# Kernel tuning notes

Measured on AMD Instinct MI355X. Metric: run time of the kernel, lower is better.

## Reference

```python
import jax, jax.numpy as jnp
import numpy as np


def setup_inputs() -> dict:
    key = jax.random.key(0)
    ks = jax.random.split(key, 9)
    b, t_q, t_k, n_q, n_k = 4, 128, 512, 512, 512
    out_size = 512
    s = 0.02  # small init scale for weights
    return {
        "query": jax.random.normal(ks[0], (b, t_q, n_q), jnp.float32),
        "keys": jax.random.normal(ks[1], (b, t_k, n_k), jnp.float32),
        "values": jax.random.normal(ks[2], (b, t_k, n_k), jnp.float32),
        "W_q": jax.random.normal(ks[3], (n_k, n_q), jnp.float32) * s,
        "b_q": jnp.zeros((n_k,), jnp.float32),
        "w_att": jax.random.normal(ks[4], (n_k,), jnp.float32) * s,
        "b_att": jnp.zeros((1,), jnp.float32),
        "W_out": jax.random.normal(ks[5], (out_size, n_q + n_k), jnp.float32) * s,
        "b_out": jnp.zeros((out_size,), jnp.float32),
    }


def reference(query, keys, values, W_q, b_q, w_att, b_att, W_out, b_out):
    # linear_q: [b, t_q, query_size] -> [b, t_q, key_size]
    att_query = jnp.einsum("bqd,nd->bqn", query, W_q) + b_q
    # Bahdanau additive score: tanh(q + k) projected by linear_att (key_size -> 1)
    # intermediate: [b, t_q, t_k, n]
    sum_qk = jnp.tanh(att_query[:, :, None, :] + keys[:, None, :, :])
    scores = jnp.einsum("bqkn,n->bqk", sum_qk, w_att) + b_att[0]
    # mask is None by default; dropout p=0 -> identity
    probs = jax.nn.softmax(scores, axis=-1)  # [b, t_q, t_k]
    context = jnp.einsum("bqk,bkn->bqn", probs, values)
    # linear_out on concat([query, context]) + tanh nonlinearity
    cat = jnp.concatenate([query, context], axis=-1)
    out = jnp.tanh(jnp.einsum("bqc,oc->bqo", cat, W_out) + b_out)
    return out, probs
```

## Files before the change

kernel.cpp:

```cpp
#include <hip/hip_runtime.h>
#include <hip/hip_fp16.h>


#define BB    4
#define TQ    128
#define TK    512
#define NN    512
#define OUTSZ 512
#define CATSZ 1024
#define K2E   2.8853900817779268f
#define L2E   1.4426950408889634f
#define MAT   262144
#define WS_HALVES (15 * MAT)

typedef __attribute__((ext_vector_type(4))) _Float16 half4;
typedef __attribute__((ext_vector_type(8))) _Float16 half8;
typedef __attribute__((ext_vector_type(2))) _Float16 h2;

#if __has_builtin(__builtin_amdgcn_exp2f)
#define EXP2F(x) __builtin_amdgcn_exp2f(x)
#else
#define EXP2F(x) exp2f(x)
#endif
#if __has_builtin(__builtin_amdgcn_rcpf)
#define RCPF(x) __builtin_amdgcn_rcpf(x)
#else
#define RCPF(x) (1.0f / (x))
#endif

__device__ __forceinline__ h2 u2h(unsigned int u) {
  union { unsigned int i; h2 h; } v; v.i = u; return v.h;
}
__device__ __forceinline__ half4 uu2h4(unsigned int a, unsigned int b) {
  union { uint2 u; half4 h; } c; c.u = make_uint2(a, b); return c.h;
}
#if __has_builtin(__builtin_amdgcn_fdot2)
__device__ __forceinline__ float FDOT2(h2 a, h2 b, float c) {
  return __builtin_amdgcn_fdot2(a, b, c, false);
}
#else
__device__ __forceinline__ float FDOT2(h2 a, h2 b, float c) {
  return fmaf((float)a.x, (float)b.x, fmaf((float)a.y, (float)b.y, c));
}
#endif

__device__ __forceinline__ float fast_tanh(float x) {
  float e = EXP2F(x * K2E);
  return fmaf(-2.0f, RCPF(e + 1.0f), 1.0f);
}
__device__ __forceinline__ float waveRedSum(float s) {
  #pragma unroll
  for (int m = 32; m >= 1; m >>= 1) s += __shfl_xor(s, m, 64);
  return s;
}
__device__ __forceinline__ float fma4(float4 w, float4 v, float acc) {
  acc = fmaf(w.x, v.x, acc); acc = fmaf(w.y, v.y, acc);
  acc = fmaf(w.z, v.z, acc); acc = fmaf(w.w, v.w, acc);
  return acc;
}
__device__ __forceinline__ float4 scqh(float4 s, half4 E, float A, float w) {
  s.x = fmaf(w, RCPF(fmaf((float)E.x, A, 1.0f)), s.x);
  s.y = fmaf(w, RCPF(fmaf((float)E.y, A, 1.0f)), s.y);
  s.z = fmaf(w, RCPF(fmaf((float)E.z, A, 1.0f)), s.z);
  s.w = fmaf(w, RCPF(fmaf((float)E.w, A, 1.0f)), s.w);
  return s;
}
__device__ __forceinline__ void dotq(float4& r0, float4& r1, uint4 wp, unsigned int cpa, unsigned int cpb) {
  h2 c0 = u2h(cpa), c1 = u2h(cpb);
  r0.x = FDOT2(u2h(wp.x), c0, r0.x); r1.x = FDOT2(u2h(wp.x), c1, r1.x);
  r0.y = FDOT2(u2h(wp.y), c0, r0.y); r1.y = FDOT2(u2h(wp.y), c1, r1.y);
  r0.z = FDOT2(u2h(wp.z), c0, r0.z); r1.z = FDOT2(u2h(wp.z), c1, r1.z);
  r0.w = FDOT2(u2h(wp.w), c0, r0.w); r1.w = FDOT2(u2h(wp.w), c1, r1.w);
}

__global__ __launch_bounds__(256)
void pack_kernel(const float* __restrict__ query,
                 const float* __restrict__ keys, const float* __restrict__ W_q,
                 const float* __restrict__ W_out, const float* __restrict__ values,
                 _Float16* __restrict__ ws)
{
  __shared__ float tile[32][33];
  const int idx = blockIdx.x;
  const int tx = threadIdx.x & 31, ty = threadIdx.x >> 5;

  if (idx >= 2816) {
    int p = idx - 2816;
    int b = (p & 7) >> 1;
    int qg = ((p >> 3) << 1) | (p & 1);
    const float* q0 = query + ((size_t)(b * TQ + qg * 2)) * NN;
    const float* q1 = q0 + NN;
    int cp = threadIdx.x;
    float2 a = *(const float2*)(q0 + 2 * cp);
    float2 c = *(const float2*)(q1 + 2 * cp);
    half4 h = {(_Float16)a.x, (_Float16)a.y, (_Float16)c.x, (_Float16)c.y};
    *(half4*)(ws + (size_t)11 * MAT + (size_t)p * 2048 + 4 * cp) = h;
    return;
  }

  if (idx >= 1792) {
    int r = idx - 1792;
    int b = r >> 8, k2 = r & 255;
    const float* r0 = values + ((size_t)b * 512 + 2 * k2) * 512;
    const float* r1 = r0 + 512;
    int n0 = threadIdx.x * 2;
    float2 a = *(const float2*)(r0 + n0);
    float2 c = *(const float2*)(r1 + n0);
    _Float16* dst = ws + (size_t)7 * MAT + (size_t)b * MAT + k2 * 1024 + n0 * 2;
    half4 h = {(_Float16)a.x, (_Float16)c.x, (_Float16)a.y, (_Float16)c.y};
    *(half4*)dst = h;
    return;
  }

  if (idx < 1024) {
    int b = idx >> 8, r = idx & 255;
    int by = r >> 4, bx = r & 15;
    const float* src = keys + (size_t)b * MAT;
    _Float16* dst = ws + (size_t)b * MAT;
    #pragma unroll
    for (int i = 0; i < 32; i += 8)
      tile[ty + i][tx] = src[(size_t)(by * 32 + ty + i) * 512 + bx * 32 + tx] * K2E;
    __syncthreads();
    #pragma unroll
    for (int i = 0; i < 32; i += 8)
      dst[(size_t)(bx * 32 + ty + i) * 512 + by * 32 + tx] = (_Float16)EXP2F(tile[tx][ty + i]);
    return;
  }

  const float* src; _Float16* dst; int N; int by, bx;
  if (idx < 1280) {
    int r = idx - 1024; by = r >> 4; bx = r & 15;
    src = W_q; dst = ws + (size_t)4 * MAT; N = 512;
  } else {
    int r = idx - 1280; by = r >> 5; bx = r & 31;
    src = W_out; dst = ws + (size_t)5 * MAT; N = 1024;
  }
  #pragma unroll
  for (int i = 0; i < 32; i += 8)
    tile[ty + i][tx] = src[(size_t)(by * 32 + ty + i) * N + bx * 32 + tx];
  __syncthreads();
  #pragma unroll
  for (int i = 0; i < 32; i += 8) {
    int d = bx * 32 + ty + i;
    int o = by * 32 + tx;
    dst[(size_t)(d >> 1) * 1024 + o * 2 + (d & 1)] = (_Float16)tile[tx][ty + i];
  }
}

__global__ __launch_bounds__(1024, 4)
void attq_kernel(const float* __restrict__ b_q, const float* __restrict__ w_att,
                 _Float16* __restrict__ ws)
{
  __shared__ __align__(16) _Float16 ldsQ[4][1024];
  __shared__ __align__(16) float pt[8][4][2][128];

  const _Float16* wsWqP = ws + (size_t)4 * MAT;
  const _Float16* catG  = ws + (size_t)11 * MAT;
  _Float16* pawG        = ws + (size_t)13 * MAT;

  const int t = threadIdx.x, bx = blockIdx.x;
  const int ng = bx & 3, pg = bx >> 2;

  if (t < 512) {
    int qp = t >> 7, j = t & 127;
    ((uint4*)&ldsQ[qp][0])[j] =
        ((const uint4*)(catG + (size_t)(4 * pg + qp) * 2048))[j];
  }
  __syncthreads();

  const int G = t >> 7, pq = (t >> 5) & 3, v5 = t & 31;
  {
    const _Float16* wq = wsWqP + 8 * (32 * ng + v5);
    float4 a0 = {0,0,0,0}, a1 = {0,0,0,0};
    #pragma unroll 2
    for (int j2 = 0; j2 < 32; j2 += 2) {
      int d2 = 32 * G + j2;
      uint4 wp0 = *(const uint4*)(wq + (size_t)d2 * 1024);
      uint4 wp1 = *(const uint4*)(wq + (size_t)(d2 + 1) * 1024);
      uint4 cp2 = *(const uint4*)(&ldsQ[pq][d2 * 4]);
      dotq(a0, a1, wp0, cp2.x, cp2.y);
      dotq(a0, a1, wp1, cp2.z, cp2.w);
    }
    *(float4*)(&pt[G][pq][0][4 * v5]) = a0;
    *(float4*)(&pt[G][pq][1][4 * v5]) = a1;
  }
  __syncthreads();
  {
    int pq2 = t >> 8, row = (t >> 7) & 1, no = t & 127;
    int n = 128 * ng + no;
    float s = pt[0][pq2][row][no] + pt[1][pq2][row][no]
            + pt[2][pq2][row][no] + pt[3][pq2][row][no]
            + pt[4][pq2][row][no] + pt[5][pq2][row][no]
            + pt[6][pq2][row][no] + pt[7][pq2][row][no];
    float A = EXP2F(K2E * (s + b_q[n]));
    _Float16* dst = pawG + (size_t)(4 * pg + pq2) * 2048 + 4 * n;
    dst[row] = (_Float16)A;
    if (row == 0) {
      dst[2] = (_Float16)w_att[n];
      dst[3] = (_Float16)0.f;
    }
  }
}

__global__ __launch_bounds__(1024, 4)
void attn_mid(_Float16* __restrict__ ws, float* __restrict__ probs)
{
  __shared__ __align__(16) _Float16 pawF[NN * 4];
  __shared__ __align__(16) _Float16 prH[1024];
  __shared__ __align__(16) float  pt[8][2][NN];
  __shared__ float reds2[2][8];

  _Float16* ptH = (_Float16*)pt;

  const _Float16* wsKeys = ws;
  const _Float16* wsValP = ws + (size_t)7 * MAT;
  _Float16* catG         = ws + (size_t)11 * MAT;
  const _Float16* pawG   = ws + (size_t)13 * MAT;

  const int t    = threadIdx.x;
  const int qh   = t >> 9;
  const int u    = t & 511;
  const int G    = t >> 7;
  const int v    = t & 127;
  const int G16  = t >> 6;
  const int v6   = t & 63;
  const int wave = t >> 6, lane = t & 63, wq8 = wave & 7;

  const int p  = blockIdx.x;
  const int b  = (p & 7) >> 1;
  const int qg = ((p >> 3) << 1) | (p & 1);
  const int qabs0 = qg * 2;

  ((unsigned int*)pawF)[t] = ((const unsigned int*)(pawG + (size_t)p * 2048))[t];
  __syncthreads();

  {
    const _Float16* ke = wsKeys + (size_t)b * MAT + 8 * v6;
    float4 s0a = {0,0,0,0}, s0b = {0,0,0,0};
    float4 s1a = {0,0,0,0}, s1b = {0,0,0,0};
    #pragma unroll 2
    for (int j = 0; j < 32; j += 2) {
      int n = 32 * G16 + j;
      uint4 Eu0 = *(const uint4*)(ke + (size_t)n * 512);
      uint4 Eu1 = *(const uint4*)(ke + (size_t)(n + 1) * 512);
      uint4 pw  = *(const uint4*)(&pawF[n * 4]);
      h2 Aab = u2h(pw.x);  float w0f = (float)u2h(pw.y).x;
      h2 Acd = u2h(pw.z);  float w1f = (float)u2h(pw.w).x;
      float A0n = (float)Aab.x, A1n = (float)Aab.y;
      float A0m = (float)Acd.x, A1m = (float)Acd.y;
      half4 E0lo = uu2h4(Eu0.x, Eu0.y), E0hi = uu2h4(Eu0.z, Eu0.w);
      half4 E1lo = uu2h4(Eu1.x, Eu1.y), E1hi = uu2h4(Eu1.z, Eu1.w);
      s0a = scqh(s0a, E0lo, A0n, w0f);
      s0b = scqh(s0b, E0hi, A0n, w0f);
      s1a = scqh(s1a, E0lo, A1n, w0f);
      s1b = scqh(s1b, E0hi, A1n, w0f);
      s0a = scqh(s0a, E1lo, A0m, w1f);
      s0b = scqh(s0b, E1hi, A0m, w1f);
      s1a = scqh(s1a, E1lo, A1m, w1f);
      s1b = scqh(s1b, E1hi, A1m, w1f);
    }
    half8 w0 = {(_Float16)s0a.x, (_Float16)s0a.y, (_Float16)s0a.z, (_Float16)s0a.w,
                (_Float16)s0b.x, (_Float16)s0b.y, (_Float16)s0b.z, (_Float16)s0b.w};
    half8 w1 = {(_Float16)s1a.x, (_Float16)s1a.y, (_Float16)s1a.z, (_Float16)s1a.w,
                (_Float16)s1b.x, (_Float16)s1b.y, (_Float16)s1b.z, (_Float16)s1b.w};
    *(half8*)(ptH + (size_t)G16 * 512 + 8 * v6)        = w0;
    *(half8*)(ptH + 8192 + (size_t)G16 * 512 + 8 * v6) = w1;
  }
  __syncthreads();

  {
    const _Float16* pp = ptH + qh * 8192 + u;
    float s = 0.f;
    #pragma unroll
    for (int g = 0; g < 16; ++g)
      s += (float)pp[g * 512];
    float e = EXP2F(-K2E * s);
    float se = waveRedSum(e);
    if (lane == 0) reds2[qh][wq8] = se;
    __syncthreads();
    float bs = reds2[qh][0]+reds2[qh][1]+reds2[qh][2]+reds2[qh][3]
             + reds2[qh][4]+reds2[qh][5]+reds2[qh][6]+reds2[qh][7];
    float pv = e * RCPF(bs);
    prH[(u >> 1) * 4 + qh * 2 + (u & 1)] = (_Float16)pv;
    probs[((size_t)(b * TQ + qabs0 + qh)) * TK + u] = pv;
  }
  __syncthreads();

  {
    const _Float16* vp = wsValP + (size_t)b * MAT + 8 * v;
    float4 c0 = {0,0,0,0}, c1 = {0,0,0,0};
    #pragma unroll 2
    for (int j2 = 0; j2 < 32; j2 += 2) {
      int k2 = 32 * G + j2;
      uint4 vk0 = *(const uint4*)(vp + (size_t)k2 * 1024);
      uint4 vk1 = *(const uint4*)(vp + (size_t)(k2 + 1) * 1024);
      uint4 pp2 = *(const uint4*)(&prH[k2 * 4]);
      dotq(c0, c1, vk0, pp2.x, pp2.y);
      dotq(c0, c1, vk1, pp2.z, pp2.w);
    }
    *(float4*)(&pt[G][0][4 * v]) = c0;
    *(float4*)(&pt[G][1][4 * v]) = c1;
  }
  __syncthreads();
  {
    float s = pt[0][qh][u] + pt[1][qh][u] + pt[2][qh][u] + pt[3][qh][u]
            + pt[4][qh][u] + pt[5][qh][u] + pt[6][qh][u] + pt[7][qh][u];
    catG[(size_t)p * 2048 + (size_t)(256 + (u >> 1)) * 4 + qh * 2 + (u & 1)] =
        (_Float16)s;
  }
}

__global__ __launch_bounds__(1024, 4)
void out_kernel(const float* __restrict__ b_out, const _Float16* __restrict__ ws,
                float* __restrict__ out)
{
  __shared__ __align__(16) _Float16 ldsCat[8192];
  __shared__ __align__(16) float pt[8][4][2][128];

  const _Float16* wsWoutP = ws + (size_t)5 * MAT;
  const _Float16* catG    = ws + (size_t)11 * MAT;

  const int t = threadIdx.x, bx = blockIdx.x;
  const int og = bx & 3, pg = bx >> 2;

  ((uint4*)ldsCat)[t] = ((const uint4*)(catG + (size_t)4 * pg * 2048))[t];
  __syncthreads();

  const int G = t >> 7, pq = (t >> 5) & 3, v5 = t & 31;
  {
    const _Float16* wo = wsWoutP + 8 * (32 * og + v5);
    float4 o0 = {0,0,0,0}, o1 = {0,0,0,0};
    #pragma unroll 2
    for (int j2 = 0; j2 < 64; j2 += 2) {
      int c2 = 64 * G + j2;
      uint4 wp0 = *(const uint4*)(wo + (size_t)c2 * 1024);
      uint4 wp1 = *(const uint4*)(wo + (size_t)(c2 + 1) * 1024);
      uint4 cp2 = *(const uint4*)(&ldsCat[pq * 2048 + c2 * 4]);
      dotq(o0, o1, wp0, cp2.x, cp2.y);
      dotq(o0, o1, wp1, cp2.z, cp2.w);
    }
    *(float4*)(&pt[G][pq][0][4 * v5]) = o0;
    *(float4*)(&pt[G][pq][1][4 * v5]) = o1;
  }
  __syncthreads();
  {
    int pq2 = t >> 8, row = (t >> 7) & 1, oo = t & 127;
    float s = pt[0][pq2][row][oo] + pt[1][pq2][row][oo]
            + pt[2][pq2][row][oo] + pt[3][pq2][row][oo]
            + pt[4][pq2][row][oo] + pt[5][pq2][row][oo]
            + pt[6][pq2][row][oo] + pt[7][pq2][row][oo];
    int o = 128 * og + oo;
    int p = 4 * pg + pq2;
    int b = (p & 7) >> 1;
    int qg = ((p >> 3) << 1) | (p & 1);
    out[((size_t)(b * TQ + qg * 2 + row)) * OUTSZ + o] = fast_tanh(s + b_out[o]);
  }
}

__device__ __forceinline__ float sc4f(float4 w, float4 k, float4 a, float acc) {
  acc = fmaf(w.x, RCPF(EXP2F(fmaf(k.x, K2E, a.x)) + 1.0f), acc);
  acc = fmaf(w.y, RCPF(EXP2F(fmaf(k.y, K2E, a.y)) + 1.0f), acc);
  acc = fmaf(w.z, RCPF(EXP2F(fmaf(k.z, K2E, a.z)) + 1.0f), acc);
  acc = fmaf(w.w, RCPF(EXP2F(fmaf(k.w, K2E, a.w)) + 1.0f), acc);
  return acc;
}

__global__ __launch_bounds__(1024, 4)
void attn_fallback(const float* __restrict__ query, const float* __restrict__ keys,
                   const float* __restrict__ values, const float* __restrict__ W_q,
                   const float* __restrict__ b_q, const float* __restrict__ w_att,
                   const float* __restrict__ b_att, const float* __restrict__ W_out,
                   const float* __restrict__ b_out,
                   float* __restrict__ out, float* __restrict__ probs)
{
  __shared__ __align__(16) float qv[2][NN];
  __shared__ __align__(16) float aqc[2][NN];
  __shared__ __align__(16) float wv[NN];
  __shared__ __align__(16) float pr[2][TK];
  __shared__ __align__(16) float ctx[2][NN];
  __shared__ __align__(16) float part[2][2][NN];
  __shared__ float redm[2][8], reds[2][8], redw[8];

  const int t = threadIdx.x, H = t >> 9, u = t & 511;
  const int wave = t >> 6, lane = t & 63, wq8 = wave & 7;
  const int p = blockIdx.x, b = (p & 7) >> 1;
  const int qg = ((p >> 3) << 1) | (p & 1), qabs0 = qg * 2;
  const float batt = b_att[0];

  if (H == 0) wv[u] = w_att[u];
  qv[H][u] = query[((size_t)(b * TQ + qabs0 + H)) * NN + u];
  __syncthreads();
  if (H == 0) {
    float wp = waveRedSum(wv[u]);
    if (lane == 0) redw[wq8] = wp;
  }
  __syncthreads();
  const float sumW = redw[0]+redw[1]+redw[2]+redw[3]+redw[4]+redw[5]+redw[6]+redw[7];

  {
    const float4* wq4 = (const float4*)(W_q + (size_t)u * NN + 256 * H);
    const float4* x4  = (const float4*)(qv[0] + 256 * H);
    const float4* y4  = (const float4*)(qv[1] + 256 * H);
    float a0=0.f, a0b=0.f, a1=0.f, a1b=0.f;
    #pragma unroll 2
    for (int c = 0; c < 16; ++c) {
      float4 wA=wq4[4*c+0], wB=wq4[4*c+1], wC=wq4[4*c+2], wD=wq4[4*c+3];
      float4 xA=x4[4*c+0], xB=x4[4*c+1], xC=x4[4*c+2], xD=x4[4*c+3];
      a0 = fma4(wA,xA,a0); a0b = fma4(wB,xB,a0b);
      a0 = fma4(wC,xC,a0); a0b = fma4(wD,xD,a0b);
      float4 yA=y4[4*c+0], yB=y4[4*c+1], yC=y4[4*c+2], yD=y4[4*c+3];
      a1 = fma4(wA,yA,a1); a1b = fma4(wB,yB,a1b);
      a1 = fma4(wC,yC,a1); a1b = fma4(wD,yD,a1b);
    }
    part[H][0][u] = a0 + a0b; part[H][1][u] = a1 + a1b;
  }
  __syncthreads();
  aqc[H][u] = (part[0][H][u] + part[1][H][u] + b_q[u]) * K2E;
  __syncthreads();

  {
    const float4* kr  = (const float4*)(keys + ((size_t)(b * TK) + u) * NN + 256 * H);
    const float4* a0p = (const float4*)(aqc[0] + 256 * H);
    const float4* a1p = (const float4*)(aqc[1] + 256 * H);
    const float4* w4  = (const float4*)(wv + 256 * H);
    float s0 = 0.f, s1 = 0.f;
    #pragma unroll 2
    for (int c = 0; c < 16; ++c) {
      float4 kA=kr[4*c+0], kB=kr[4*c+1], kC=kr[4*c+2], kD=kr[4*c+3];
      float4 wA=w4[4*c+0], wB=w4[4*c+1], wC=w4[4*c+2], wD=w4[4*c+3];
      float4 aA=a0p[4*c+0], aB=a0p[4*c+1], aC=a0p[4*c+2], aD=a0p[4*c+3];
      s0 = sc4f(wA,kA,aA,s0); s0 = sc4f(wB,kB,aB,s0);
      s0 = sc4f(wC,kC,aC,s0); s0 = sc4f(wD,kD,aD,s0);
      float4 bA=a1p[4*c+0], bB=a1p[4*c+1], bC=a1p[4*c+2], bD=a1p[4*c+3];
      s1 = sc4f(wA,kA,bA,s1); s1 = sc4f(wB,kB,bB,s1);
      s1 = sc4f(wC,kC,bC,s1); s1 = sc4f(wD,kD,bD,s1);
    }
    part[H][0][u] = s0; part[H][1][u] = s1;
  }
  __syncthreads();

  {
    float sc = batt + sumW - 2.0f * (part[0][H][u] + part[1][H][u]);
    float m = sc;
    #pragma unroll
    for (int mm = 32; mm >= 1; mm >>= 1) m = fmaxf(m, __shfl_xor(m, mm, 64));
    if (lane == 0) redm[H][wq8] = m;
    __syncthreads();
    float bm = fmaxf(fmaxf(fmaxf(redm[H][0],redm[H][1]),fmaxf(redm[H][2],redm[H][3])),
                     fmaxf(fmaxf(redm[H][4],redm[H][5]),fmaxf(redm[H][6],redm[H][7])));
    float e = EXP2F((sc - bm) * L2E);
    float se = waveRedSum(e);
    if (lane == 0) reds[H][wq8] = se;
    __syncthreads();
    float bs = reds[H][0]+reds[H][1]+reds[H][2]+reds[H][3]
             + reds[H][4]+reds[H][5]+reds[H][6]+reds[H][7];
    float pv = e * RCPF(bs);
    pr[H][u] = pv;
    probs[((size_t)(b * TQ + qabs0 + H)) * TK + u] = pv;
  }
  __syncthreads();

  {
    const float* vcol = values + ((size_t)(b * TK) + 256 * H) * NN + u;
    const float4* p0 = (const float4*)(pr[0] + 256 * H);
    const float4* p1 = (const float4*)(pr[1] + 256 * H);
    float c0a=0.f, c0b=0.f, c1a=0.f, c1b=0.f;
    #pragma unroll 2
    for (int k = 0; k < 256; k += 8) {
      float v0 = vcol[(size_t)(k+0)*NN]; float v1 = vcol[(size_t)(k+1)*NN];
      float v2 = vcol[(size_t)(k+2)*NN]; float v3 = vcol[(size_t)(k+3)*NN];
      float v4 = vcol[(size_t)(k+4)*NN]; float v5 = vcol[(size_t)(k+5)*NN];
      float v6 = vcol[(size_t)(k+6)*NN]; float v7 = vcol[(size_t)(k+7)*NN];
      float4 pA = p0[k>>2], pB = p0[(k>>2)+1];
      float4 qA = p1[k>>2], qB = p1[(k>>2)+1];
      c0a = fmaf(pA.x,v0,c0a); c0a = fmaf(pA.y,v1,c0a);
      c0b = fmaf(pA.z,v2,c0b); c0b = fmaf(pA.w,v3,c0b);
      c0a = fmaf(pB.x,v4,c0a); c0a = fmaf(pB.y,v5,c0a);
      c0b = fmaf(pB.z,v6,c0b); c0b = fmaf(pB.w,v7,c0b);
      c1a = fmaf(qA.x,v0,c1a); c1a = fmaf(qA.y,v1,c1a);
      c1b = fmaf(qA.z,v2,c1b); c1b = fmaf(qA.w,v3,c1b);
      c1a = fmaf(qB.x,v4,c1a); c1a = fmaf(qB.y,v5,c1a);
      c1b = fmaf(qB.z,v6,c1b); c1b = fmaf(qB.w,v7,c1b);
    }
    part[H][0][u] = c0a + c0b; part[H][1][u] = c1a + c1b;
  }
  __syncthreads();
  ctx[H][u] = part[0][H][u] + part[1][H][u];
  __syncthreads();

  {
    const float4* wo = (const float4*)(W_out + (size_t)u * CATSZ + 512 * H);
    const float4* x4 = (H == 0) ? (const float4*)qv[0] : (const float4*)ctx[0];
    const float4* y4 = (H == 0) ? (const float4*)qv[1] : (const float4*)ctx[1];
    float o0=0.f, o0b=0.f, o1=0.f, o1b=0.f;
    #pragma unroll 2
    for (int c = 0; c < 32; ++c) {
      float4 wA=wo[4*c+0], wB=wo[4*c+1], wC=wo[4*c+2], wD=wo[4*c+3];
      float4 xA=x4[4*c+0], xB=x4[4*c+1], xC=x4[4*c+2], xD=x4[4*c+3];
      o0 = fma4(wA,xA,o0); o0b = fma4(wB,xB,o0b);
      o0 = fma4(wC,xC,o0); o0b = fma4(wD,xD,o0b);
      float4 yA=y4[4*c+0], yB=y4[4*c+1], yC=y4[4*c+2], yD=y4[4*c+3];
      o1 = fma4(wA,yA,o1); o1b = fma4(wB,yB,o1b);
      o1 = fma4(wC,yC,o1); o1b = fma4(wD,yD,o1b);
    }
    part[H][0][u] = o0 + o0b; part[H][1][u] = o1 + o1b;
  }
  __syncthreads();
  {
    float oo = part[0][H][u] + part[1][H][u] + b_out[u];
    out[((size_t)(b * TQ + qabs0 + H)) * OUTSZ + u] = fast_tanh(oo);
  }
}

extern "C" void kernel_launch(void* const* d_in, const int* in_sizes, int n_in,
                              void* d_out, int out_size, void* d_ws, size_t ws_size,
                              hipStream_t stream) {
  const float* query = (const float*)d_in[0];
  const float* keys  = (const float*)d_in[1];
  const float* vals  = (const float*)d_in[2];
  const float* W_q   = (const float*)d_in[3];
  const float* b_q   = (const float*)d_in[4];
  const float* w_att = (const float*)d_in[5];
  const float* b_att = (const float*)d_in[6];
  const float* W_out = (const float*)d_in[7];
  const float* b_out = (const float*)d_in[8];

  float* out   = (float*)d_out;
  float* probs = out + (size_t)BB * TQ * OUTSZ;

  if (ws_size >= (size_t)WS_HALVES * sizeof(_Float16)) {
    _Float16* ws = (_Float16*)d_ws;
    pack_kernel<<<dim3(3072), dim3(256), 0, stream>>>(query, keys, W_q, W_out, vals, ws);
    attq_kernel<<<dim3(256), dim3(1024), 0, stream>>>(b_q, w_att, ws);
    attn_mid<<<dim3(BB * TQ / 2), dim3(1024), 0, stream>>>(ws, probs);
    out_kernel<<<dim3(256), dim3(1024), 0, stream>>>(b_out, ws, out);
  } else {
    attn_fallback<<<dim3(BB * TQ / 2), dim3(1024), 0, stream>>>(
        query, keys, vals, W_q, b_q, w_att, b_att, W_out, b_out, out, probs);
  }
}
```

Measured before the change: 118.1 us.

## Fold query projection into pack kernel, drop separate attq launch

Computes the att_query projection, its exp2 transform and the w_att packing directly inside the pack kernel in fp32 from raw W_q and query. This removes the W_q transpose/packing blocks and the separate attq_kernel launch. Block index ranges are remapped so the projection blocks come first. Each projection block rereads W_q rows from global memory in fp32, which adds memory traffic.

```diff
diff --git a/kernel.cpp b/kernel.cpp
--- a/kernel.cpp
+++ b/kernel.cpp
@@ -77,11 +77,62 @@
 void pack_kernel(const float* __restrict__ query,
                  const float* __restrict__ keys, const float* __restrict__ W_q,
                  const float* __restrict__ W_out, const float* __restrict__ values,
+                 const float* __restrict__ b_q, const float* __restrict__ w_att,
                  _Float16* __restrict__ ws)
 {
-  __shared__ float tile[32][33];
+  __shared__ __align__(16) float smem[8 * 512];
+  float (*tile)[33] = (float (*)[33])smem;
+  float (*qlds)[512] = (float (*)[512])smem;
+
   const int idx = blockIdx.x;
   const int tx = threadIdx.x & 31, ty = threadIdx.x >> 5;
+
+  if (idx < 256) {
+    {
+      int i = threadIdx.x >> 5;
+      int d0 = (threadIdx.x & 31) * 16;
+      int p = 4 * (idx >> 2) + (i >> 1);
+      int bb = (p & 7) >> 1;
+      int qg = ((p >> 3) << 1) | (p & 1);
+      const float4* qr =
+          (const float4*)(query + ((size_t)(bb * TQ + qg * 2 + (i & 1))) * NN + d0);
+      float4* dst4 = (float4*)&qlds[i][d0];
+      dst4[0] = qr[0]; dst4[1] = qr[1]; dst4[2] = qr[2]; dst4[3] = qr[3];
+    }
+    __syncthreads();
+    const int ng = idx & 3, pg = idx >> 2;
+    const int n = 128 * ng + (threadIdx.x & 127);
+    const int rh = threadIdx.x >> 7;
+    const float4* wr = (const float4*)(W_q + (size_t)n * NN);
+    const float4* q0 = (const float4*)qlds[4 * rh + 0];
+    const float4* q1 = (const float4*)qlds[4 * rh + 1];
+    const float4* q2 = (const float4*)qlds[4 * rh + 2];
+    const float4* q3 = (const float4*)qlds[4 * rh + 3];
+    float a0 = 0.f, a1 = 0.f, a2 = 0.f, a3 = 0.f;
+    #pragma unroll 4
+    for (int d4 = 0; d4 < 128; ++d4) {
+      float4 w4 = wr[d4];
+      a0 = fma4(w4, q0[d4], a0);
+      a1 = fma4(w4, q1[d4], a1);
+      a2 = fma4(w4, q2[d4], a2);
+      a3 = fma4(w4, q3[d4], a3);
+    }
+    float bq = b_q[n], wa = w_att[n];
+    _Float16* pawG = ws + (size_t)13 * MAT;
+    {
+      float A0 = EXP2F(K2E * (a0 + bq));
+      float A1 = EXP2F(K2E * (a1 + bq));
+      half4 h = {(_Float16)A0, (_Float16)A1, (_Float16)wa, (_Float16)0.f};
+      *(half4*)(pawG + (size_t)(4 * pg + 2 * rh) * 2048 + 4 * n) = h;
+    }
+    {
+      float A0 = EXP2F(K2E * (a2 + bq));
+      float A1 = EXP2F(K2E * (a3 + bq));
+      half4 h = {(_Float16)A0, (_Float16)A1, (_Float16)wa, (_Float16)0.f};
+      *(half4*)(pawG + (size_t)(4 * pg + 2 * rh + 1) * 2048 + 4 * n) = h;
+    }
+    return;
+  }
 
   if (idx >= 2816) {
     int p = idx - 2816;
@@ -97,8 +148,8 @@
     return;
   }
 
-  if (idx >= 1792) {
-    int r = idx - 1792;
+  if (idx >= 1280 && idx < 2304) {
+    int r = idx - 1280;
     int b = r >> 8, k2 = r & 255;
     const float* r0 = values + ((size_t)b * 512 + 2 * k2) * 512;
     const float* r1 = r0 + 512;
@@ -111,8 +162,9 @@
     return;
   }
 
-  if (idx < 1024) {
-    int b = idx >> 8, r = idx & 255;
+  if (idx < 1280) {
+    int r2 = idx - 256;
+    int b = r2 >> 8, r = r2 & 255;
     int by = r >> 4, bx = r & 15;
     const float* src = keys + (size_t)b * MAT;
     _Float16* dst = ws + (size_t)b * MAT;
@@ -126,77 +178,20 @@
     return;
   }
 
-  const float* src; _Float16* dst; int N; int by, bx;
-  if (idx < 1280) {
-    int r = idx - 1024; by = r >> 4; bx = r & 15;
-    src = W_q; dst = ws + (size_t)4 * MAT; N = 512;
-  } else {
-    int r = idx - 1280; by = r >> 5; bx = r & 31;
-    src = W_out; dst = ws + (size_t)5 * MAT; N = 1024;
-  }
-  #pragma unroll
-  for (int i = 0; i < 32; i += 8)
-    tile[ty + i][tx] = src[(size_t)(by * 32 + ty + i) * N + bx * 32 + tx];
-  __syncthreads();
-  #pragma unroll
-  for (int i = 0; i < 32; i += 8) {
-    int d = bx * 32 + ty + i;
-    int o = by * 32 + tx;
-    dst[(size_t)(d >> 1) * 1024 + o * 2 + (d & 1)] = (_Float16)tile[tx][ty + i];
-  }
-}
-
-__global__ __launch_bounds__(1024, 4)
-void attq_kernel(const float* __restrict__ b_q, const float* __restrict__ w_att,
-                 _Float16* __restrict__ ws)
-{
-  __shared__ __align__(16) _Float16 ldsQ[4][1024];
-  __shared__ __align__(16) float pt[8][4][2][128];
-
-  const _Float16* wsWqP = ws + (size_t)4 * MAT;
-  const _Float16* catG  = ws + (size_t)11 * MAT;
-  _Float16* pawG        = ws + (size_t)13 * MAT;
-
-  const int t = threadIdx.x, bx = blockIdx.x;
-  const int ng = bx & 3, pg = bx >> 2;
-
-  if (t < 512) {
-    int qp = t >> 7, j = t & 127;
-    ((uint4*)&ldsQ[qp][0])[j] =
-        ((const uint4*)(catG + (size_t)(4 * pg + qp) * 2048))[j];
-  }
-  __syncthreads();
-
-  const int G = t >> 7, pq = (t >> 5) & 3, v5 = t & 31;
-  {
-    const _Float16* wq = wsWqP + 8 * (32 * ng + v5);
-    float4 a0 = {0,0,0,0}, a1 = {0,0,0,0};
-    #pragma unroll 2
-    for (int j2 = 0; j2 < 32; j2 += 2) {
-      int d2 = 32 * G + j2;
-      uint4 wp0 = *(const uint4*)(wq + (size_t)d2 * 1024);
-      uint4 wp1 = *(const uint4*)(wq + (size_t)(d2 + 1) * 1024);
-      uint4 cp2 = *(const uint4*)(&ldsQ[pq][d2 * 4]);
-      dotq(a0, a1, wp0, cp2.x, cp2.y);
-      dotq(a0, a1, wp1, cp2.z, cp2.w);
-    }
-    *(float4*)(&pt[G][pq][0][4 * v5]) = a0;
-    *(float4*)(&pt[G][pq][1][4 * v5]) = a1;
-  }
-  __syncthreads();
-  {
-    int pq2 = t >> 8, row = (t >> 7) & 1, no = t & 127;
-    int n = 128 * ng + no;
-    float s = pt[0][pq2][row][no] + pt[1][pq2][row][no]
-            + pt[2][pq2][row][no] + pt[3][pq2][row][no]
-            + pt[4][pq2][row][no] + pt[5][pq2][row][no]
-            + pt[6][pq2][row][no] + pt[7][pq2][row][no];
-    float A = EXP2F(K2E * (s + b_q[n]));
-    _Float16* dst = pawG + (size_t)(4 * pg + pq2) * 2048 + 4 * n;
-    dst[row] = (_Float16)A;
-    if (row == 0) {
-      dst[2] = (_Float16)w_att[n];
-      dst[3] = (_Float16)0.f;
+  {
+    int r = idx - 2304;
+    int by = r >> 5, bx = r & 31;
+    const float* src = W_out;
+    _Float16* dst = ws + (size_t)5 * MAT;
+    #pragma unroll
+    for (int i = 0; i < 32; i += 8)
+      tile[ty + i][tx] = src[(size_t)(by * 32 + ty + i) * 1024 + bx * 32 + tx];
+    __syncthreads();
+    #pragma unroll
+    for (int i = 0; i < 32; i += 8) {
+      int d = bx * 32 + ty + i;
+      int o = by * 32 + tx;
+      dst[(size_t)(d >> 1) * 1024 + o * 2 + (d & 1)] = (_Float16)tile[tx][ty + i];
     }
   }
 }
@@ -529,8 +524,8 @@
 
   if (ws_size >= (size_t)WS_HALVES * sizeof(_Float16)) {
     _Float16* ws = (_Float16*)d_ws;
-    pack_kernel<<<dim3(3072), dim3(256), 0, stream>>>(query, keys, W_q, W_out, vals, ws);
-    attq_kernel<<<dim3(256), dim3(1024), 0, stream>>>(b_q, w_att, ws);
+    pack_kernel<<<dim3(3072), dim3(256), 0, stream>>>(query, keys, W_q, W_out,
+                                                      vals, b_q, w_att, ws);
     attn_mid<<<dim3(BB * TQ / 2), dim3(1024), 0, stream>>>(ws, probs);
     out_kernel<<<dim3(256), dim3(1024), 0, stream>>>(b_out, ws, out);
   } else {
```

Measured after the change: 127.3 us. 7.8% more time.
